# Performance work log

Measured on AMD Instinct MI355X. Metric: run time of the kernel, lower is better.

Reference implementation:

```python
import jax, jax.numpy as jnp
import numpy as np

H, W = 96, 96
SIGMA_PX = 1.5
ZMIN, ZMAX = 0.2, 10.0
FX = FY = 60.0


def setup_inputs() -> dict:
    key = jax.random.key(0)
    k1, k2 = jax.random.split(key)
    B, K, N = 4, 8, 256
    # x,y spread so projections land around the image; z inside z_clip
    xy = jax.random.normal(k1, (B, K, N, 2), dtype=jnp.float32) * 1.5
    z = jax.random.uniform(k2, (B, K, N, 1), dtype=jnp.float32, minval=0.5, maxval=5.0)
    points_world = jnp.concatenate([xy, z], axis=-1)  # (B,K,N,3)
    return {"points_world": points_world}


def reference(points_world):
    # points_world: (B,K,N,3) -> image (B,1,H,W)
    dt = points_world.dtype
    cx = (W - 1) / 2.0
    cy = (H - 1) / 2.0
    x = points_world[..., 0]
    y = points_world[..., 1]
    z = jnp.maximum(points_world[..., 2], 0.001)
    valid = ((z > ZMIN) & (z < ZMAX)).astype(dt)  # (B,K,N)
    u = FX * (x / z) + cx  # (B,K,N)
    v = FY * (y / z) + cy
    gx = jnp.arange(W, dtype=dt)  # pixel x coords
    gy = jnp.arange(H, dtype=dt)  # pixel y coords
    # Isotropic Gaussian is separable: exp(-0.5*(dx^2+dy^2)) = ex * ey
    ex = jnp.exp(-0.5 * ((gx[None, None, None, :] - u[..., None]) / SIGMA_PX) ** 2)  # (B,K,N,W)
    ey = jnp.exp(-0.5 * ((gy[None, None, None, :] - v[..., None]) / SIGMA_PX) ** 2)  # (B,K,N,H)
    ey = ey * valid[..., None]
    # sum over K and N point splats -> (B,H,W)
    img = jnp.einsum('bknh,bknw->bhw', ey, ex)
    img = 1.0 - jnp.exp(-img)
    return img[:, None, :, :]  # (B,1,H,W)
```

## Files before the change

### kernel.cpp

```cpp
#include <hip/hip_runtime.h>
#include <hip/hip_bf16.h>


#define HDIM 96
#define WDIM 96
#define PIX   (HDIM * WDIM)
#define PTS_PER_BATCH 2048
#define P_CHUNK 64
#define CHUNKS  32
#define BATCHES 4
#define NPART   (BATCHES * CHUNKS)

__global__ __launch_bounds__(256)
void splat_partial_kernel(const float* __restrict__ pts, float* __restrict__ ws) {
    __shared__ float sex[P_CHUNK][WDIM];
    __shared__ float sey[P_CHUNK][HDIM];
    __shared__ float su[P_CHUNK], sv[P_CHUNK];

    const int b = blockIdx.x >> 5;
    const int c = blockIdx.x & (CHUNKS - 1);
    const int t = threadIdx.x;

    if (t < P_CHUNK) {
        const int p = (b * PTS_PER_BATCH + c * P_CHUNK + t) * 3;
        const float x = pts[p + 0];
        const float y = pts[p + 1];
        float z = fmaxf(pts[p + 2], 0.001f);
        const bool valid = (z > 0.2f && z < 10.0f);
        const float inv = __frcp_rn(z);
        su[t] = 60.0f * x * inv + 47.5f;
        sv[t] = valid ? (60.0f * y * inv + 47.5f) : 1.0e9f;
    }
    __syncthreads();

    const float kcoef = -1.0f / (2.0f * 1.5f * 1.5f);
    for (int i = t; i < P_CHUNK * 96; i += 256) {
        const int p = i / 96;
        const int cidx = i - p * 96;
        const float fc = (float)cidx;
        const float du = fc - su[p];
        const float dv = fc - sv[p];
        sex[p][cidx] = __expf(kcoef * du * du);
        sey[p][cidx] = __expf(kcoef * dv * dv);
    }
    __syncthreads();

    const int tw = t & 7;
    const int th = t >> 3;
    const int w0 = tw * 12;
    const int h0 = th * 3;

    float acc[3][12];
#pragma unroll
    for (int i = 0; i < 3; ++i)
#pragma unroll
        for (int j = 0; j < 12; ++j) acc[i][j] = 0.0f;

#pragma unroll
    for (int p = 0; p < P_CHUNK; ++p) {
        const float4* exv = (const float4*)&sex[p][w0];
        const float4 e0 = exv[0], e1 = exv[1], e2 = exv[2];
        const float ex[12] = { e0.x, e0.y, e0.z, e0.w, e1.x, e1.y, e1.z, e1.w,
                               e2.x, e2.y, e2.z, e2.w };
        float ey[3];
#pragma unroll
        for (int i = 0; i < 3; ++i) ey[i] = sey[p][h0 + i];
#pragma unroll
        for (int i = 0; i < 3; ++i)
#pragma unroll
            for (int j = 0; j < 12; ++j) acc[i][j] = fmaf(ey[i], ex[j], acc[i][j]);
    }

    float* base = ws + (size_t)blockIdx.x * PIX;
#pragma unroll
    for (int i = 0; i < 3; ++i) {
        float4* dst = (float4*)&base[(h0 + i) * WDIM + w0];
#pragma unroll
        for (int q = 0; q < 3; ++q)
            dst[q] = make_float4(acc[i][4*q+0], acc[i][4*q+1], acc[i][4*q+2], acc[i][4*q+3]);
    }
}

__global__ __launch_bounds__(256)
void reduce_finish_kernel(const float* __restrict__ ws, float* __restrict__ out) {
    const int g = blockIdx.x * 256 + threadIdx.x;
    const int b = g / PIX;
    const int i = g - b * PIX;

    const float* src = ws + (size_t)b * CHUNKS * PIX + i;

    float s0 = 0.f, s1 = 0.f, s2 = 0.f, s3 = 0.f;
#pragma unroll
    for (int c = 0; c < CHUNKS; c += 4) {
        s0 += src[(size_t)(c + 0) * PIX];
        s1 += src[(size_t)(c + 1) * PIX];
        s2 += src[(size_t)(c + 2) * PIX];
        s3 += src[(size_t)(c + 3) * PIX];
    }
    const float s = (s0 + s1) + (s2 + s3);
    out[g] = 1.0f - __expf(-s);
}

extern "C" void kernel_launch(void* const* d_in, const int* in_sizes, int n_in,
                              void* d_out, int out_size, void* d_ws, size_t ws_size,
                              hipStream_t stream) {
    const float* pts = (const float*)d_in[0];
    float* ws  = (float*)d_ws;
    float* out = (float*)d_out;

    splat_partial_kernel<<<NPART, 256, 0, stream>>>(pts, ws);
    reduce_finish_kernel<<<(BATCHES * PIX) / 256, 256, 0, stream>>>(ws, out);
}
```

Baseline: 62.88 us.

## Split splat blocks by image half and store partial sums in fp16

The splat kernel now launches twice as many blocks, each covering half of the image rows with a smaller 3x6 per-thread tile. Each block computes only the ey values for its own half. Partial sums go to the workspace as half2 instead of float4, which halves the workspace traffic. The reduce kernel now handles two pixels per thread and accumulates in fp32. The cost is fp16 rounding in the partials and recomputing ex in both halves.

Measured after the change: 61.28 us (median of 2 runs). -2.5%, faster.

```diff
diff --git a/kernel.cpp b/kernel.cpp
--- a/kernel.cpp
+++ b/kernel.cpp
@@ -1,10 +1,11 @@
 #include <hip/hip_runtime.h>
-#include <hip/hip_bf16.h>
+#include <hip/hip_fp16.h>
 
 
 #define HDIM 96
 #define WDIM 96
 #define PIX   (HDIM * WDIM)
+#define HHALF 48
 #define PTS_PER_BATCH 2048
 #define P_CHUNK 64
 #define CHUNKS  32
@@ -12,13 +13,14 @@
 #define NPART   (BATCHES * CHUNKS)
 
 __global__ __launch_bounds__(256)
-void splat_partial_kernel(const float* __restrict__ pts, float* __restrict__ ws) {
+void splat_partial_kernel(const float* __restrict__ pts, __half* __restrict__ ws) {
     __shared__ float sex[P_CHUNK][WDIM];
-    __shared__ float sey[P_CHUNK][HDIM];
+    __shared__ float sey[P_CHUNK][HHALF];
     __shared__ float su[P_CHUNK], sv[P_CHUNK];
 
-    const int b = blockIdx.x >> 5;
-    const int c = blockIdx.x & (CHUNKS - 1);
+    const int b    = blockIdx.x >> 6;
+    const int c    = (blockIdx.x >> 1) & (CHUNKS - 1);
+    const int half = blockIdx.x & 1;
     const int t = threadIdx.x;
 
     if (t < P_CHUNK) {
@@ -34,80 +36,92 @@
     __syncthreads();
 
     const float kcoef = -1.0f / (2.0f * 1.5f * 1.5f);
-    for (int i = t; i < P_CHUNK * 96; i += 256) {
-        const int p = i / 96;
-        const int cidx = i - p * 96;
-        const float fc = (float)cidx;
-        const float du = fc - su[p];
-        const float dv = fc - sv[p];
+    const float rowbase = (float)(half * HHALF);
+    for (int i = t; i < P_CHUNK * WDIM; i += 256) {
+        const int p = i / WDIM;
+        const int cidx = i - p * WDIM;
+        const float du = (float)cidx - su[p];
         sex[p][cidx] = __expf(kcoef * du * du);
-        sey[p][cidx] = __expf(kcoef * dv * dv);
+    }
+    for (int i = t; i < P_CHUNK * HHALF; i += 256) {
+        const int p = i / HHALF;
+        const int r = i - p * HHALF;
+        const float dv = rowbase + (float)r - sv[p];
+        sey[p][r] = __expf(kcoef * dv * dv);
     }
     __syncthreads();
 
-    const int tw = t & 7;
-    const int th = t >> 3;
-    const int w0 = tw * 12;
-    const int h0 = th * 3;
+    const int tw = t & 15;
+    const int th = t >> 4;
+    const int w0 = tw * 6;
+    const int r0 = th * 3;
 
-    float acc[3][12];
+    float acc[3][6];
 #pragma unroll
     for (int i = 0; i < 3; ++i)
 #pragma unroll
-        for (int j = 0; j < 12; ++j) acc[i][j] = 0.0f;
+        for (int j = 0; j < 6; ++j) acc[i][j] = 0.0f;
 
 #pragma unroll
     for (int p = 0; p < P_CHUNK; ++p) {
-        const float4* exv = (const float4*)&sex[p][w0];
-        const float4 e0 = exv[0], e1 = exv[1], e2 = exv[2];
-        const float ex[12] = { e0.x, e0.y, e0.z, e0.w, e1.x, e1.y, e1.z, e1.w,
-                               e2.x, e2.y, e2.z, e2.w };
+        const float2 e0 = *(const float2*)&sex[p][w0 + 0];
+        const float2 e1 = *(const float2*)&sex[p][w0 + 2];
+        const float2 e2 = *(const float2*)&sex[p][w0 + 4];
+        const float ex[6] = { e0.x, e0.y, e1.x, e1.y, e2.x, e2.y };
         float ey[3];
 #pragma unroll
-        for (int i = 0; i < 3; ++i) ey[i] = sey[p][h0 + i];
+        for (int i = 0; i < 3; ++i) ey[i] = sey[p][r0 + i];
 #pragma unroll
         for (int i = 0; i < 3; ++i)
 #pragma unroll
-            for (int j = 0; j < 12; ++j) acc[i][j] = fmaf(ey[i], ex[j], acc[i][j]);
+            for (int j = 0; j < 6; ++j) acc[i][j] = fmaf(ey[i], ex[j], acc[i][j]);
     }
 
-    float* base = ws + (size_t)blockIdx.x * PIX;
+    const int part = b * CHUNKS + c;
+    __half* base = ws + (size_t)part * PIX;
 #pragma unroll
     for (int i = 0; i < 3; ++i) {
-        float4* dst = (float4*)&base[(h0 + i) * WDIM + w0];
+        __half2* dst = (__half2*)&base[(half * HHALF + r0 + i) * WDIM + w0];
 #pragma unroll
         for (int q = 0; q < 3; ++q)
-            dst[q] = make_float4(acc[i][4*q+0], acc[i][4*q+1], acc[i][4*q+2], acc[i][4*q+3]);
+            dst[q] = __floats2half2_rn(acc[i][2*q + 0], acc[i][2*q + 1]);
     }
 }
 
 __global__ __launch_bounds__(256)
-void reduce_finish_kernel(const float* __restrict__ ws, float* __restrict__ out) {
+void reduce_finish_kernel(const __half2* __restrict__ ws, float2* __restrict__ out) {
     const int g = blockIdx.x * 256 + threadIdx.x;
-    const int b = g / PIX;
-    const int i = g - b * PIX;
+    const int b = g / (PIX / 2);
+    const int i = g - b * (PIX / 2);
 
-    const float* src = ws + (size_t)b * CHUNKS * PIX + i;
+    const __half2* src = ws + (size_t)b * CHUNKS * (PIX / 2) + i;
 
-    float s0 = 0.f, s1 = 0.f, s2 = 0.f, s3 = 0.f;
+    float2 s0 = make_float2(0.f, 0.f), s1 = s0, s2 = s0, s3 = s0;
 #pragma unroll
     for (int c = 0; c < CHUNKS; c += 4) {
-        s0 += src[(size_t)(c + 0) * PIX];
-        s1 += src[(size_t)(c + 1) * PIX];
-        s2 += src[(size_t)(c + 2) * PIX];
-        s3 += src[(size_t)(c + 3) * PIX];
+        const float2 v0 = __half22float2(src[(size_t)(c + 0) * (PIX / 2)]);
+        const float2 v1 = __half22float2(src[(size_t)(c + 1) * (PIX / 2)]);
+        const float2 v2 = __half22float2(src[(size_t)(c + 2) * (PIX / 2)]);
+        const float2 v3 = __half22float2(src[(size_t)(c + 3) * (PIX / 2)]);
+        s0.x += v0.x; s0.y += v0.y;
+        s1.x += v1.x; s1.y += v1.y;
+        s2.x += v2.x; s2.y += v2.y;
+        s3.x += v3.x; s3.y += v3.y;
     }
-    const float s = (s0 + s1) + (s2 + s3);
-    out[g] = 1.0f - __expf(-s);
+    const float sx = (s0.x + s1.x) + (s2.x + s3.x);
+    const float sy = (s0.y + s1.y) + (s2.y + s3.y);
+
+    out[g] = make_float2(1.0f - __expf(-sx), 1.0f - __expf(-sy));
 }
 
 extern "C" void kernel_launch(void* const* d_in, const int* in_sizes, int n_in,
                               void* d_out, int out_size, void* d_ws, size_t ws_size,
                               hipStream_t stream) {
     const float* pts = (const float*)d_in[0];
-    float* ws  = (float*)d_ws;
-    float* out = (float*)d_out;
+    __half* ws = (__half*)d_ws;
+    float2* out = (float2*)d_out;
 
-    splat_partial_kernel<<<NPART, 256, 0, stream>>>(pts, ws);
-    reduce_finish_kernel<<<(BATCHES * PIX) / 256, 256, 0, stream>>>(ws, out);
+    splat_partial_kernel<<<NPART * 2, 256, 0, stream>>>(pts, ws);
+    reduce_finish_kernel<<<(BATCHES * PIX / 2) / 256, 256, 0, stream>>>(
+        (const __half2*)ws, out);
 }
```
